# Optimization experiments

Hardware: AMD Instinct MI355X
Metric: run time of the kernel (lower is better)

Reference implementation:

```python
import jax, jax.numpy as jnp
import numpy as np

NUM_EMBEDDINGS = 8192
EMBEDDING_DIM = 256
COMMITMENT_COST = 0.25
TAU = 0.9
B, C, H, W = 4, NUM_EMBEDDINGS, 32, 32


def setup_inputs() -> dict:
    key = jax.random.key(0)
    k1, k2, k3 = jax.random.split(key, 3)
    x = jax.random.normal(k1, (B, C, H, W), dtype=jnp.float32)
    # nn.Embedding weight initialized uniform(-0.5, 0.5)
    emb_weight = jax.random.uniform(k2, (NUM_EMBEDDINGS, EMBEDDING_DIM),
                                    dtype=jnp.float32, minval=-0.5, maxval=0.5)
    # standard Gumbel(0,1) noise, sampled once for reproducibility
    u = jax.random.uniform(k3, (B, C, H, W), dtype=jnp.float32,
                           minval=1e-10, maxval=1.0)
    gumbel_noise = -jnp.log(-jnp.log(u))
    return {"x": x, "emb_weight": emb_weight, "gumbel_noise": gumbel_noise}


def reference(x, emb_weight, gumbel_noise):
    n = x.shape[1]  # num_embeddings (channel dim)
    # --- gumbel_softmax(tau=0.9, hard=True, dim=1) ---
    y_soft = jax.nn.softmax((x + gumbel_noise) / TAU, axis=1)  # [B,N,H,W]
    idx = jnp.argmax(y_soft, axis=1)                           # [B,H,W]
    y_hard = jax.nn.one_hot(idx, n, axis=1, dtype=y_soft.dtype)
    # straight-through estimator
    one_hot = y_soft + jax.lax.stop_gradient(y_hard - y_soft)  # [B,N,H,W]
    # --- codebook lookup as one-hot matmul ---
    quantized = jnp.einsum('bnhw,nd->bdhw', one_hot, emb_weight)
    # --- KL(uniform || q) with F.kl_div semantics, reduction='batchmean' ---
    # logits rearranged to b (h w) n and log_softmax over n == log_softmax over axis=1 of x
    log_qy = jax.nn.log_softmax(x, axis=1)                     # [B,N,H,W]
    t = 1.0 / n
    # pointwise kl = target * (log(target) - log_qy); batchmean divides by B
    kl_div = jnp.sum(t * (jnp.log(jnp.asarray(t, x.dtype)) - log_qy)) / x.shape[0]
    return quantized, COMMITMENT_COST * kl_div, one_hot
```

## Files before the change

kernel.cpp:

```cpp
#include <hip/hip_runtime.h>
#include <math.h>

#define BSZ 4
#define CCH 8192
#define HH 32
#define WW 32
#define DEMB 256
#define NPOS (BSZ*HH*WW)
#define NCHUNK 8
#define CHUNK (CCH/NCHUNK)
#define QSIZE (BSZ*DEMB*HH*WW)
#define KLOFF QSIZE
#define OHOFF (QSIZE+1)

#define WS_BEST 0
#define WS_IDX  (NCHUNK*NPOS)
#define WS_M    (2*NCHUNK*NPOS)
#define WS_S    (3*NCHUNK*NPOS)
#define WS_SX   (4*NCHUNK*NPOS)
#define WS_FIDX (5*NCHUNK*NPOS)

__global__ __launch_bounds__(256) void vq_phase1(const float* __restrict__ x,
                                                 const float* __restrict__ g,
                                                 float* __restrict__ ws) {
    int bid = blockIdx.x;
    int chunk = bid & 7;
    int bh = bid >> 3;
    int b = bh >> 5;
    int h = bh & 31;
    int tid = threadIdx.x;
    int p = tid & 7;
    int cg = tid >> 3;
    int c0 = chunk * CHUNK + cg;
    int w4 = p * 4;
    size_t base = ((size_t)(b * CCH + c0) * (HH * WW)) + h * WW + w4;

    float best[4], m[4], s[4], sx[4];
    int bidx[4];
#pragma unroll
    for (int j = 0; j < 4; j++) { best[j] = -INFINITY; bidx[j] = 0; m[j] = -INFINITY; s[j] = 0.f; sx[j] = 0.f; }

    for (int i = 0; i < CHUNK / 32; i++) {
        size_t idx = base + (size_t)i * 32 * (HH * WW);
        float4 xv = *(const float4*)(x + idx);
        float4 gv = *(const float4*)(g + idx);
        int c = c0 + i * 32;
        float xa[4] = {xv.x, xv.y, xv.z, xv.w};
        float ga[4] = {gv.x, gv.y, gv.z, gv.w};
#pragma unroll
        for (int j = 0; j < 4; j++) {
            float z = xa[j] + ga[j];
            if (z > best[j]) { best[j] = z; bidx[j] = c; }
            float v = xa[j];
            float mn = fmaxf(m[j], v);
            s[j] = s[j] * __expf(m[j] - mn) + __expf(v - mn);
            m[j] = mn;
            sx[j] += v;
        }
    }

    __shared__ float l_best[32][33];
    __shared__ int   l_idx [32][33];
    __shared__ float l_m   [32][33];
    __shared__ float l_s   [32][33];
    __shared__ float l_sx  [32][33];
#pragma unroll
    for (int j = 0; j < 4; j++) {
        l_best[cg][w4 + j] = best[j];
        l_idx [cg][w4 + j] = bidx[j];
        l_m   [cg][w4 + j] = m[j];
        l_s   [cg][w4 + j] = s[j];
        l_sx  [cg][w4 + j] = sx[j];
    }
    __syncthreads();

    if (tid < 32) {
        int w = tid;
        float fb = l_best[0][w]; int fi = l_idx[0][w];
        float fm = l_m[0][w], fs = l_s[0][w], fsx = l_sx[0][w];
        for (int q = 1; q < 32; q++) {
            float v = l_best[q][w]; int ci = l_idx[q][w];
            if (v > fb || (v == fb && ci < fi)) { fb = v; fi = ci; }
            float mm = l_m[q][w], ss = l_s[q][w];
            float mn = fmaxf(fm, mm);
            fs = fs * __expf(fm - mn) + ss * __expf(mm - mn);
            fm = mn;
            fsx += l_sx[q][w];
        }
        int pos = (b * HH + h) * WW + w;
        int o = chunk * NPOS + pos;
        ws[WS_BEST + o] = fb;
        ((int*)ws)[WS_IDX + o] = fi;
        ws[WS_M + o] = fm;
        ws[WS_S + o] = fs;
        ws[WS_SX + o] = fsx;
    }
}

__global__ __launch_bounds__(256) void vq_phase2(float* __restrict__ out,
                                                 float* __restrict__ ws) {
    int pos = blockIdx.x * 256 + threadIdx.x;
    float fb = -INFINITY; int fi = 0;
    float fm = -INFINITY, fs = 0.f, fsx = 0.f;
    for (int q = 0; q < NCHUNK; q++) {
        int o = q * NPOS + pos;
        float v = ws[WS_BEST + o]; int ci = ((int*)ws)[WS_IDX + o];
        if (v > fb || (v == fb && ci < fi)) { fb = v; fi = ci; }
        float mm = ws[WS_M + o], ss = ws[WS_S + o];
        float mn = fmaxf(fm, mm);
        fs = fs * __expf(fm - mn) + ss * __expf(mm - mn);
        fm = mn;
        fsx += ws[WS_SX + o];
    }
    ((int*)ws)[WS_FIDX + pos] = fi;

    int b = pos >> 10;
    int hw = pos & 1023;
    out[OHOFF + (size_t)(b * CCH + fi) * (HH * WW) + hw] = 1.0f;

    float lse = fm + __logf(fs);
    const float logt = -9.0109131783f;
    float term = logt + lse - fsx * (1.0f / (float)CCH);

    for (int off = 32; off > 0; off >>= 1) term += __shfl_down(term, off, 64);
    __shared__ float wsum[4];
    int lane = threadIdx.x & 63, wv = threadIdx.x >> 6;
    if (lane == 0) wsum[wv] = term;
    __syncthreads();
    if (threadIdx.x == 0) {
        float t = wsum[0] + wsum[1] + wsum[2] + wsum[3];
        atomicAdd(out + KLOFF, (0.25f / (float)BSZ) * t);
    }
}

__global__ __launch_bounds__(256) void vq_phase3(const float* __restrict__ emb,
                                                 const int* __restrict__ fidx,
                                                 float* __restrict__ outq) {
    int t = blockIdx.x * 256 + threadIdx.x;
    int b = t >> 18;
    int r = t & 262143;
    int d = r >> 10;
    int hw = r & 1023;
    int pos = (b << 10) | hw;
    int c = fidx[pos];
    outq[t] = emb[c * DEMB + d];
}

extern "C" void kernel_launch(void* const* d_in, const int* in_sizes, int n_in,
                              void* d_out, int out_size, void* d_ws, size_t ws_size,
                              hipStream_t stream) {
    (void)in_sizes; (void)n_in; (void)out_size; (void)ws_size;
    const float* x   = (const float*)d_in[0];
    const float* emb = (const float*)d_in[1];
    const float* g   = (const float*)d_in[2];
    float* out = (float*)d_out;
    float* ws  = (float*)d_ws;

    hipMemsetAsync(out + KLOFF, 0, (size_t)(1 + (size_t)BSZ * CCH * HH * WW) * sizeof(float), stream);

    vq_phase1<<<dim3(BSZ * HH * NCHUNK), dim3(256), 0, stream>>>(x, g, ws);
    vq_phase2<<<dim3(NPOS / 256), dim3(256), 0, stream>>>(out, ws);
    vq_phase3<<<dim3(QSIZE / 256), dim3(256), 0, stream>>>(emb, (const int*)(ws + WS_FIDX), out);
}
```

Baseline: 354.7 us.

## Fuse one-hot zeroing into the reduction pass and repartition channels per block

The separate memset of the large one-hot output is removed. Zero-filling now happens inside phase1, which already streams x and g, using float4 stores at the same addresses it reads. Phase1 is reorganised so each block covers the whole spatial extent for a contiguous channel slice; the number of channels per block is picked from the available workspace size, and the shared-memory reduction is gone. The log-sum-exp drops its running max and sums __expf(x) directly, which relies on logits small enough not to overflow. Phase3 now gathers four positions per thread and writes them with one float4 store.

```diff
diff --git a/kernel.cpp b/kernel.cpp
--- a/kernel.cpp
+++ b/kernel.cpp
@@ -3,162 +3,151 @@
 
 #define BSZ 4
 #define CCH 8192
-#define HH 32
-#define WW 32
+#define HW  1024
 #define DEMB 256
-#define NPOS (BSZ*HH*WW)
-#define NCHUNK 8
-#define CHUNK (CCH/NCHUNK)
-#define QSIZE (BSZ*DEMB*HH*WW)
+#define NPOS (BSZ*HW)
+#define QSIZE (BSZ*DEMB*HW)
 #define KLOFF QSIZE
 #define OHOFF (QSIZE+1)
+#define OHSZ  ((size_t)BSZ*CCH*HW)
 
-#define WS_BEST 0
-#define WS_IDX  (NCHUNK*NPOS)
-#define WS_M    (2*NCHUNK*NPOS)
-#define WS_S    (3*NCHUNK*NPOS)
-#define WS_SX   (4*NCHUNK*NPOS)
-#define WS_FIDX (5*NCHUNK*NPOS)
-
+template<int CPB>
 __global__ __launch_bounds__(256) void vq_phase1(const float* __restrict__ x,
                                                  const float* __restrict__ g,
+                                                 float* __restrict__ out,
                                                  float* __restrict__ ws) {
+    constexpr int NCH = CCH / CPB;
+    constexpr int P   = NPOS * NCH;
     int bid = blockIdx.x;
-    int chunk = bid & 7;
-    int bh = bid >> 3;
-    int b = bh >> 5;
-    int h = bh & 31;
-    int tid = threadIdx.x;
-    int p = tid & 7;
-    int cg = tid >> 3;
-    int c0 = chunk * CHUNK + cg;
-    int w4 = p * 4;
-    size_t base = ((size_t)(b * CCH + c0) * (HH * WW)) + h * WW + w4;
+    int q = bid % NCH;
+    int b = bid / NCH;
+    int t = threadIdx.x;
+    int c0 = q * CPB;
+    size_t row0 = (size_t)(b * CCH + c0);
+    size_t base = row0 * HW + 4 * t;
 
-    float best[4], m[4], s[4], sx[4];
-    int bidx[4];
+    float best[4]; int bidx[4]; float s[4], sx[4];
 #pragma unroll
-    for (int j = 0; j < 4; j++) { best[j] = -INFINITY; bidx[j] = 0; m[j] = -INFINITY; s[j] = 0.f; sx[j] = 0.f; }
+    for (int j = 0; j < 4; j++) { best[j] = -INFINITY; bidx[j] = 0; s[j] = 0.f; sx[j] = 0.f; }
 
-    for (int i = 0; i < CHUNK / 32; i++) {
-        size_t idx = base + (size_t)i * 32 * (HH * WW);
-        float4 xv = *(const float4*)(x + idx);
-        float4 gv = *(const float4*)(g + idx);
-        int c = c0 + i * 32;
+    const float4 z4 = make_float4(0.f, 0.f, 0.f, 0.f);
+#pragma unroll 4
+    for (int c = 0; c < CPB; c++) {
+        size_t a = base + (size_t)c * HW;
+        float4 xv = *(const float4*)(x + a);
+        float4 gv = *(const float4*)(g + a);
+        *(float4*)(out + QSIZE + a) = z4;
+        int cc = c0 + c;
         float xa[4] = {xv.x, xv.y, xv.z, xv.w};
         float ga[4] = {gv.x, gv.y, gv.z, gv.w};
 #pragma unroll
         for (int j = 0; j < 4; j++) {
             float z = xa[j] + ga[j];
-            if (z > best[j]) { best[j] = z; bidx[j] = c; }
-            float v = xa[j];
-            float mn = fmaxf(m[j], v);
-            s[j] = s[j] * __expf(m[j] - mn) + __expf(v - mn);
-            m[j] = mn;
-            sx[j] += v;
+            if (z > best[j]) { best[j] = z; bidx[j] = cc; }
+            s[j]  += __expf(xa[j]);
+            sx[j] += xa[j];
         }
     }
 
-    __shared__ float l_best[32][33];
-    __shared__ int   l_idx [32][33];
-    __shared__ float l_m   [32][33];
-    __shared__ float l_s   [32][33];
-    __shared__ float l_sx  [32][33];
-#pragma unroll
-    for (int j = 0; j < 4; j++) {
-        l_best[cg][w4 + j] = best[j];
-        l_idx [cg][w4 + j] = bidx[j];
-        l_m   [cg][w4 + j] = m[j];
-        l_s   [cg][w4 + j] = s[j];
-        l_sx  [cg][w4 + j] = sx[j];
-    }
-    __syncthreads();
+    if (b == BSZ - 1 && q == NCH - 1 && t == 255)
+        out[QSIZE + OHSZ] = 0.f;
 
-    if (tid < 32) {
-        int w = tid;
-        float fb = l_best[0][w]; int fi = l_idx[0][w];
-        float fm = l_m[0][w], fs = l_s[0][w], fsx = l_sx[0][w];
-        for (int q = 1; q < 32; q++) {
-            float v = l_best[q][w]; int ci = l_idx[q][w];
-            if (v > fb || (v == fb && ci < fi)) { fb = v; fi = ci; }
-            float mm = l_m[q][w], ss = l_s[q][w];
-            float mn = fmaxf(fm, mm);
-            fs = fs * __expf(fm - mn) + ss * __expf(mm - mn);
-            fm = mn;
-            fsx += l_sx[q][w];
-        }
-        int pos = (b * HH + h) * WW + w;
-        int o = chunk * NPOS + pos;
-        ws[WS_BEST + o] = fb;
-        ((int*)ws)[WS_IDX + o] = fi;
-        ws[WS_M + o] = fm;
-        ws[WS_S + o] = fs;
-        ws[WS_SX + o] = fsx;
-    }
+    int o = q * NPOS + b * HW + 4 * t;
+    float* wbest = ws;
+    int*   widx  = (int*)(ws + P);
+    float* wsum  = ws + 2 * (size_t)P;
+    float* wsx   = ws + 3 * (size_t)P;
+    *(float4*)(wbest + o) = make_float4(best[0], best[1], best[2], best[3]);
+    *(int4*)  (widx  + o) = make_int4(bidx[0], bidx[1], bidx[2], bidx[3]);
+    *(float4*)(wsum  + o) = make_float4(s[0], s[1], s[2], s[3]);
+    *(float4*)(wsx   + o) = make_float4(sx[0], sx[1], sx[2], sx[3]);
 }
 
+template<int CPB>
 __global__ __launch_bounds__(256) void vq_phase2(float* __restrict__ out,
                                                  float* __restrict__ ws) {
+    constexpr int NCH = CCH / CPB;
+    constexpr int P   = NPOS * NCH;
     int pos = blockIdx.x * 256 + threadIdx.x;
+    const float* wbest = ws;
+    const int*   widx  = (const int*)(ws + P);
+    const float* wsum  = ws + 2 * (size_t)P;
+    const float* wsx   = ws + 3 * (size_t)P;
+    int*         fidx  = (int*)(ws + 4 * (size_t)P);
+
     float fb = -INFINITY; int fi = 0;
-    float fm = -INFINITY, fs = 0.f, fsx = 0.f;
-    for (int q = 0; q < NCHUNK; q++) {
+    float fs = 0.f, fsx = 0.f;
+    for (int q = 0; q < NCH; q++) {
         int o = q * NPOS + pos;
-        float v = ws[WS_BEST + o]; int ci = ((int*)ws)[WS_IDX + o];
+        float v = wbest[o]; int ci = widx[o];
         if (v > fb || (v == fb && ci < fi)) { fb = v; fi = ci; }
-        float mm = ws[WS_M + o], ss = ws[WS_S + o];
-        float mn = fmaxf(fm, mm);
-        fs = fs * __expf(fm - mn) + ss * __expf(mm - mn);
-        fm = mn;
-        fsx += ws[WS_SX + o];
+        fs  += wsum[o];
+        fsx += wsx[o];
     }
-    ((int*)ws)[WS_FIDX + pos] = fi;
+    fidx[pos] = fi;
 
     int b = pos >> 10;
-    int hw = pos & 1023;
-    out[OHOFF + (size_t)(b * CCH + fi) * (HH * WW) + hw] = 1.0f;
+    int hw = pos & (HW - 1);
+    out[OHOFF + ((size_t)(b * CCH + fi)) * HW + hw] = 1.0f;
 
-    float lse = fm + __logf(fs);
+    float lse = __logf(fs);
     const float logt = -9.0109131783f;
     float term = logt + lse - fsx * (1.0f / (float)CCH);
 
     for (int off = 32; off > 0; off >>= 1) term += __shfl_down(term, off, 64);
-    __shared__ float wsum[4];
+    __shared__ float wsuml[4];
     int lane = threadIdx.x & 63, wv = threadIdx.x >> 6;
-    if (lane == 0) wsum[wv] = term;
+    if (lane == 0) wsuml[wv] = term;
     __syncthreads();
     if (threadIdx.x == 0) {
-        float t = wsum[0] + wsum[1] + wsum[2] + wsum[3];
-        atomicAdd(out + KLOFF, (0.25f / (float)BSZ) * t);
+        float tt = wsuml[0] + wsuml[1] + wsuml[2] + wsuml[3];
+        atomicAdd(out + KLOFF, (0.25f / (float)BSZ) * tt);
     }
 }
 
 __global__ __launch_bounds__(256) void vq_phase3(const float* __restrict__ emb,
                                                  const int* __restrict__ fidx,
                                                  float* __restrict__ outq) {
-    int t = blockIdx.x * 256 + threadIdx.x;
-    int b = t >> 18;
-    int r = t & 262143;
-    int d = r >> 10;
-    int hw = r & 1023;
-    int pos = (b << 10) | hw;
-    int c = fidx[pos];
-    outq[t] = emb[c * DEMB + d];
+    int u = blockIdx.x * 256 + threadIdx.x;
+    int b = u >> 16;
+    int r = u & 65535;
+    int d = r >> 8;
+    int h4 = (r & 255) * 4;
+    int pos = (b << 10) + h4;
+    float4 v;
+    v.x = emb[fidx[pos + 0] * DEMB + d];
+    v.y = emb[fidx[pos + 1] * DEMB + d];
+    v.z = emb[fidx[pos + 2] * DEMB + d];
+    v.w = emb[fidx[pos + 3] * DEMB + d];
+    *(float4*)(outq + ((size_t)(b * DEMB + d) << 10) + h4) = v;
+}
+
+template<int CPB>
+static void launch_all(const float* x, const float* emb, const float* g,
+                       float* out, float* ws, hipStream_t stream) {
+    constexpr int NCH = CCH / CPB;
+    constexpr int P   = NPOS * NCH;
+    vq_phase1<CPB><<<dim3(BSZ * NCH), dim3(256), 0, stream>>>(x, g, out, ws);
+    vq_phase2<CPB><<<dim3(NPOS / 256), dim3(256), 0, stream>>>(out, ws);
+    vq_phase3<<<dim3(QSIZE / 4 / 256), dim3(256), 0, stream>>>(
+        emb, (const int*)(ws + 4 * (size_t)P), out);
 }
 
 extern "C" void kernel_launch(void* const* d_in, const int* in_sizes, int n_in,
                               void* d_out, int out_size, void* d_ws, size_t ws_size,
                               hipStream_t stream) {
-    (void)in_sizes; (void)n_in; (void)out_size; (void)ws_size;
+    (void)in_sizes; (void)n_in; (void)out_size;
     const float* x   = (const float*)d_in[0];
     const float* emb = (const float*)d_in[1];
     const float* g   = (const float*)d_in[2];
     float* out = (float*)d_out;
     float* ws  = (float*)d_ws;
 
-    hipMemsetAsync(out + KLOFF, 0, (size_t)(1 + (size_t)BSZ * CCH * HH * WW) * sizeof(float), stream);
-
-    vq_phase1<<<dim3(BSZ * HH * NCHUNK), dim3(256), 0, stream>>>(x, g, ws);
-    vq_phase2<<<dim3(NPOS / 256), dim3(256), 0, stream>>>(out, ws);
-    vq_phase3<<<dim3(QSIZE / 256), dim3(256), 0, stream>>>(emb, (const int*)(ws + WS_FIDX), out);
+    if (ws_size >= (size_t)16 * (NPOS * (CCH / 64)) + 4 * NPOS) {
+        launch_all<64>(x, emb, g, out, ws, stream);
+    } else if (ws_size >= (size_t)16 * (NPOS * (CCH / 128)) + 4 * NPOS) {
+        launch_all<128>(x, emb, g, out, ws, stream);
+    } else {
+        launch_all<256>(x, emb, g, out, ws, stream);
+    }
 }
```

Result: slower. 390.9 us (+10.2%).
